# Kernel tuning notes

Measured on AMD Instinct MI355X. Metric: run time of the kernel, lower is better.

The kernel has to match this reference:

```python
import jax, jax.numpy as jnp
import numpy as np
import math

MODEL_DIM = 1024
BATCH = 4
SEQ = 4096
ATTENTION_INPUT = 'both'


def make_F(model_dim, attention_input):
    F = jnp.zeros((model_dim, model_dim), dtype=jnp.float32)
    if attention_input == 'both':
        a = model_dim
    else:
        a = model_dim // 2
    # faithful to source: elif means 'both' only hits the first branch
    if attention_input in ['both', 'only_sem']:
        idx = jnp.arange(0, a)
        F = F.at[idx, idx].set(1.0)
    elif attention_input in ['only_pos']:
        idx = jnp.arange(a, 2 * a)
        F = F.at[idx, idx].set(1.0)
    return F


def setup_inputs() -> dict:
    key = jax.random.key(0)
    kx, kq, kk, kv = jax.random.split(key, 4)
    x = jax.random.normal(kx, (BATCH, SEQ, MODEL_DIM), dtype=jnp.float32)
    Q = jax.random.normal(kq, (MODEL_DIM, MODEL_DIM), dtype=jnp.float32) / math.sqrt(MODEL_DIM)
    K = jax.random.normal(kk, (MODEL_DIM, MODEL_DIM), dtype=jnp.float32) / math.sqrt(MODEL_DIM)
    V = jax.random.normal(kv, (MODEL_DIM, MODEL_DIM), dtype=jnp.float32) / math.sqrt(MODEL_DIM)
    return {"x": x, "Q": Q, "K": K, "V": V}


def reference(x, Q, K, V):
    model_dim = Q.shape[0]
    F = make_F(model_dim, ATTENTION_INPUT)
    Qx = x @ F @ Q            # [B, S, D]
    Kx = x @ F @ K            # [B, S, D]
    Vx = x @ V                # [B, S, D]
    scores = jnp.einsum('bqd,bkd->bqk', Qx, Kx) / math.sqrt(model_dim)  # [B, S, S]
    seq = x.shape[1]
    causal_mask = jnp.triu(jnp.ones((seq, seq), dtype=bool), k=1)       # True above diagonal
    scores = jnp.where(causal_mask, -jnp.inf, scores)
    probs = jax.nn.softmax(scores, axis=-1)
    return jnp.einsum('bqk,bkd->bqd', probs, Vx)
```

## Files before the change

### kernel.cpp

```cpp
#include <hip/hip_runtime.h>
#include <cstdint>
#include <cstddef>
#include <cmath>


typedef unsigned short u16;
typedef __bf16  bf16x8 __attribute__((ext_vector_type(8)));
typedef float   f32x4  __attribute__((ext_vector_type(4)));
typedef unsigned short u16x4 __attribute__((ext_vector_type(4)));
typedef unsigned short u16x8 __attribute__((ext_vector_type(8)));

typedef __attribute__((address_space(1))) void gvoid;
typedef __attribute__((address_space(3))) void lvoid;

__device__ __forceinline__ u16 f2bf(float f) {
  union { float f; unsigned u; } v; v.f = f;
  unsigned u = v.u;
  u += 0x7FFFu + ((u >> 16) & 1u);
  return (u16)(u >> 16);
}
__device__ __forceinline__ float bf2f(u16 h) {
  union { unsigned u; float f; } v; v.u = ((unsigned)h) << 16;
  return v.f;
}
__device__ __forceinline__ void async16(const void* g, void* l) {
  __builtin_amdgcn_global_load_lds((gvoid*)(void*)g, (lvoid*)l, 16, 0, 0);
}

__global__ void __launch_bounds__(256) cvt_f32_bf16(const float4* __restrict__ in,
                                                    u16* __restrict__ out, int n4) {
  int i = blockIdx.x * 256 + threadIdx.x;
  if (i >= n4) return;
  float4 v = in[i];
  u16x4 o = { f2bf(v.x), f2bf(v.y), f2bf(v.z), f2bf(v.w) };
  *(u16x4*)(out + 4 * (size_t)i) = o;
}

template <typename TIN>
__global__ void __launch_bounds__(256) transpose_to_bf16(
    const TIN* __restrict__ in, u16* __restrict__ out,
    int rows, int cols, long inStride, long outStride, float scale) {
  __shared__ u16 t[64][68];
  int rt = blockIdx.x * 64, ct = blockIdx.y * 64;
  long ib = (long)blockIdx.z * inStride, ob = (long)blockIdx.z * outStride;
  int tx = threadIdx.x & 63, ty = threadIdx.x >> 6;
#pragma unroll
  for (int r = ty; r < 64; r += 4)
    t[r][tx] = f2bf((float)in[ib + (long)(rt + r) * cols + ct + tx] * scale);
  __syncthreads();
#pragma unroll
  for (int r = ty; r < 64; r += 4)
    out[ob + (long)(ct + r) * rows + rt + tx] = t[tx][r];
}


#define G8_BAR()  __builtin_amdgcn_s_barrier()
#define G8_VMC4() asm volatile("s_waitcnt vmcnt(4)" ::: "memory")
#define G8_VMC0() asm volatile("s_waitcnt vmcnt(0)" ::: "memory")

#define G8_STAGE_A(bn, kp, kb) do { \
    async16(Ag + (kb) + a0, (void*)&As[bn][kp][l0]); \
    async16(Ag + (kb) + a1, (void*)&As[bn][kp][l1]); } while (0)
#define G8_STAGE_B(bn, kp, kb) do { \
    async16(Bg + (kb) + b0, (void*)&Bs[bn][kp][l0]); \
    async16(Bg + (kb) + b1, (void*)&Bs[bn][kp][l1]); } while (0)

#define G8_LDA(bc, kp, ch) do { _Pragma("unroll") \
    for (int u_ = 0; u_ < 4; ++u_) \
      af[u_] = *(const bf16x8*)&As[bc][kp][(wm * 128 + (ch) * 64 + u_ * 16 + lr) * 32 + swq]; \
  } while (0)
#define G8_LDB(bc, kp) do { _Pragma("unroll") \
    for (int j_ = 0; j_ < 4; ++j_) \
      bf[j_] = *(const bf16x8*)&Bs[bc][kp][(wn * 64 + j_ * 16 + lr) * 32 + swq]; \
  } while (0)

#define G8_MFMA(ch) do { \
    __builtin_amdgcn_s_setprio(1); \
    _Pragma("unroll") for (int u_ = 0; u_ < 4; ++u_) \
      _Pragma("unroll") for (int j_ = 0; j_ < 4; ++j_) \
        acc[(ch) * 4 + u_][j_] = __builtin_amdgcn_mfma_f32_16x16x32_bf16( \
            af[u_], bf[j_], acc[(ch) * 4 + u_][j_], 0, 0, 0); \
    __builtin_amdgcn_s_setprio(0); } while (0)

#define G8_TILE(bc, bn, kt, kn) do { \
    bf16x8 af[4], bf[4]; \
     \
    G8_LDB(bc, 0); G8_LDA(bc, 0, 0); \
    G8_STAGE_A(bn, 0, (kn)); \
    G8_BAR(); G8_MFMA(0); G8_BAR(); \
     \
    G8_LDA(bc, 0, 1); \
    G8_STAGE_B(bn, 0, (kn)); \
    G8_BAR(); G8_MFMA(1); G8_VMC4(); G8_BAR(); \
     \
    G8_LDB(bc, 1); G8_LDA(bc, 1, 0); \
    G8_STAGE_A(bn, 1, (kn) + 32); \
    G8_BAR(); G8_MFMA(0); G8_BAR(); \
     \
    G8_LDA(bc, 1, 1); \
    G8_STAGE_B(bn, 1, (kn) + 32); \
    G8_BAR(); G8_MFMA(1); G8_VMC4(); G8_BAR(); } while (0)

template <bool OUTF32, bool TRI>
__global__ void __launch_bounds__(512, 2) gemm8_bt(
    const u16* __restrict__ A, const u16* __restrict__ Bt, void* __restrict__ C,
    int K, int lda, int ldb, int ldc,
    long aStride, long bStride, long cStride, float alpha) {
  int mt, nt;
  if (TRI) {
    const int bid = blockIdx.x;
    int m = (int)((sqrtf(8.0f * (float)bid + 1.0f) - 1.0f) * 0.5f);
    while ((m + 1) * (m + 2) / 2 <= bid) ++m;
    while (m * (m + 1) / 2 > bid) --m;
    mt = m; nt = bid - m * (m + 1) / 2;
  } else { mt = blockIdx.x; nt = blockIdx.y; }
  const int bz = blockIdx.z;
  const int tid = threadIdx.x, wv = tid >> 6, ln = tid & 63;
  const int wm = wv & 1, wn = wv >> 1;
  const int lr = ln & 15, quad = ln >> 4;
  const int swq = (quad ^ ((lr >> 1) & 3)) << 3;
  const u16* Ag = A + (long)bz * aStride + (long)(mt * 256) * lda;
  const u16* Bg = Bt + (long)bz * bStride + (long)(nt * 256) * ldb;

  __shared__ __align__(16) __bf16 As[2][2][256 * 32];
  __shared__ __align__(16) __bf16 Bs[2][2][256 * 32];

  f32x4 acc[8][4];
#pragma unroll
  for (int i = 0; i < 8; ++i)
#pragma unroll
    for (int j = 0; j < 4; ++j)
#pragma unroll
      for (int r = 0; r < 4; ++r) acc[i][j][r] = 0.f;

  const int c0 = tid, c1 = tid + 512;
  const int r0 = c0 >> 2, r1 = c1 >> 2;
  const long a0 = (long)r0 * lda + (((c0 & 3) ^ ((r0 >> 1) & 3)) << 3);
  const long a1 = (long)r1 * lda + (((c1 & 3) ^ ((r1 >> 1) & 3)) << 3);
  const long b0 = (long)r0 * ldb + (((c0 & 3) ^ ((r0 >> 1) & 3)) << 3);
  const long b1 = (long)r1 * ldb + (((c1 & 3) ^ ((r1 >> 1) & 3)) << 3);
  const int l0 = c0 * 8, l1 = c1 * 8;

  const int kend = K;

  G8_STAGE_A(0, 0, 0); G8_STAGE_B(0, 0, 0);
  G8_STAGE_A(0, 1, 32); G8_STAGE_B(0, 1, 32);
  G8_VMC4(); G8_BAR();

  for (int k0 = 0; k0 < kend; k0 += 128) {
    const long kn0 = (k0 + 64  < kend) ? (long)k0 + 64  : (long)k0;
    const long kn1 = (k0 + 128 < kend) ? (long)k0 + 128 : (long)k0 + 64;
    G8_TILE(0, 1, k0, kn0);
    G8_TILE(1, 0, k0 + 64, kn1);
  }
  G8_VMC0();

  const long cb = (long)bz * cStride;
#pragma unroll
  for (int i = 0; i < 8; ++i) {
    int row0 = mt * 256 + wm * 128 + i * 16 + quad * 4;
#pragma unroll
    for (int j = 0; j < 4; ++j) {
      int col = nt * 256 + wn * 64 + j * 16 + lr;
#pragma unroll
      for (int r = 0; r < 4; ++r) {
        float v = acc[i][j][r] * alpha;
        long idx = cb + (long)(row0 + r) * ldc + col;
        if (OUTF32) ((float*)C)[idx] = v;
        else        ((u16*)C)[idx]  = f2bf(v);
      }
    }
  }
}

template <bool OUTF32, bool TRI, bool CK, int BM>
__global__ void __launch_bounds__(256, BM == 256 ? 2 : 4) gemm_bt(
    const u16* __restrict__ A, const u16* __restrict__ Bt, void* __restrict__ C,
    int K, int lda, int ldb, int ldc,
    long aStride, long bStride, long cStride, float alpha) {
  constexpr int MR = BM / 32;
  constexpr int AQ = BM / 64;
  int mt, nt, bz;
  if (TRI) {
    const int bid = blockIdx.x;
    int m = (int)((sqrtf(4.0f * (float)bid + 1.0f) - 1.0f) * 0.5f);
    while ((m + 1) * (m + 2) <= bid) ++m;
    while (m * (m + 1) > bid) --m;
    mt = m; nt = bid - m * (m + 1);
    bz = blockIdx.z;
  } else if (CK) {
    const int id = blockIdx.x;
    const int g = id & 7, mid = (id >> 3) & 31, hi = id >> 8;
    bz = mid & 3; nt = mid >> 2;
    mt = (hi == 0) ? 31 - g : (hi == 1) ? 16 + g : (hi == 2) ? 15 - g : g;
  } else {
    mt = blockIdx.x; nt = blockIdx.y; bz = blockIdx.z;
  }
  const int tid = threadIdx.x, wv = tid >> 6, ln = tid & 63;
  const u16* Ag = A + (long)bz * aStride + (long)(mt * BM) * lda;
  const u16* Bg = Bt + (long)bz * bStride + (long)(nt * 128) * ldb;

  __shared__ __align__(16) __bf16 As[2][BM * 32];
  __shared__ __align__(16) __bf16 Bs[2][128 * 32];

  f32x4 acc[MR][4];
#pragma unroll
  for (int i = 0; i < MR; ++i)
#pragma unroll
    for (int j = 0; j < 4; ++j)
#pragma unroll
      for (int r = 0; r < 4; ++r) acc[i][j][r] = 0.f;

  const int kend = CK ? (((mt + 1) * BM < K) ? (mt + 1) * BM : K) : K;
  const int wm = wv & 1, wn = wv >> 1;
  const int mrow = wm * (BM / 2), nrow = wn * 64;
  const int lr = ln & 15, quad = ln >> 4;

  long aOff[AQ]; int aLds[AQ];
#pragma unroll
  for (int q = 0; q < AQ; ++q) {
    int c = q * 256 + tid, row = c >> 2, c8i = c & 3;
    aOff[q] = (long)row * lda + ((c8i ^ ((row >> 1) & 3)) << 3);
    aLds[q] = c * 8;
  }
  long bOff[2]; int bLds[2];
#pragma unroll
  for (int q = 0; q < 2; ++q) {
    int c = q * 256 + tid, row = c >> 2, c8i = c & 3;
    bOff[q] = (long)row * ldb + ((c8i ^ ((row >> 1) & 3)) << 3);
    bLds[q] = c * 8;
  }
  const int swq = (quad ^ ((lr >> 1) & 3)) << 3;

  for (int k0 = 0; k0 < kend; k0 += 64) {
#pragma unroll
    for (int p = 0; p < 2; ++p) {
      const long kk = k0 + p * 32;
#pragma unroll
      for (int q = 0; q < AQ; ++q)
        async16(Ag + kk + aOff[q], (char*)As[p] + aLds[q] * 2);
#pragma unroll
      for (int q = 0; q < 2; ++q)
        async16(Bg + kk + bOff[q], (char*)Bs[p] + bLds[q] * 2);
    }
    __syncthreads();
#pragma unroll
    for (int p = 0; p < 2; ++p) {
      bf16x8 af[MR], bfr[4];
#pragma unroll
      for (int u = 0; u < MR; ++u)
        af[u] = *(const bf16x8*)&As[p][(mrow + u * 16 + lr) * 32 + swq];
#pragma unroll
      for (int j = 0; j < 4; ++j)
        bfr[j] = *(const bf16x8*)&Bs[p][(nrow + j * 16 + lr) * 32 + swq];
#pragma unroll
      for (int u = 0; u < MR; ++u)
#pragma unroll
        for (int j = 0; j < 4; ++j)
          acc[u][j] = __builtin_amdgcn_mfma_f32_16x16x32_bf16(af[u], bfr[j], acc[u][j], 0, 0, 0);
    }
    __syncthreads();
  }

  const long cb = (long)bz * cStride;
#pragma unroll
  for (int i = 0; i < MR; ++i) {
    int row0 = mt * BM + mrow + i * 16 + quad * 4;
#pragma unroll
    for (int j = 0; j < 4; ++j) {
      int col = nt * 128 + nrow + j * 16 + lr;
#pragma unroll
      for (int r = 0; r < 4; ++r) {
        float v = acc[i][j][r] * alpha;
        long idx = cb + (long)(row0 + r) * ldc + col;
        if (OUTF32) ((float*)C)[idx] = v;
        else        ((u16*)C)[idx]  = f2bf(v);
      }
    }
  }
}

__global__ void __launch_bounds__(256) softmax_rows(u16* __restrict__ Sb,
                                                    long bStride, int S) {
  const int row = blockIdx.x;
  u16* p = Sb + (long)blockIdx.y * bStride + (long)row * S;
  const int L = row + 1;
  const int Lpad = (L + 255) & ~255;
  const int tid = threadIdx.x, ln = tid & 63, wv = tid >> 6;
  const int base0 = tid * 16;
  __shared__ float red[4];

  float vals[16];
  float lmax = -3.4e38f;
#pragma unroll
  for (int k = 0; k < 2; ++k) {
    const int b = base0 + k * 8;
    if (b < L) {
      u16x8 v = *(const u16x8*)(p + b);
#pragma unroll
      for (int e = 0; e < 8; ++e) {
        if (b + e < L) { float f = bf2f(v[e]); vals[k * 8 + e] = f; lmax = fmaxf(lmax, f); }
        else vals[k * 8 + e] = 0.f;
      }
    } else {
#pragma unroll
      for (int e = 0; e < 8; ++e) vals[k * 8 + e] = 0.f;
    }
  }
#pragma unroll
  for (int o = 32; o > 0; o >>= 1) lmax = fmaxf(lmax, __shfl_down(lmax, o));
  if (ln == 0) red[wv] = lmax;
  __syncthreads();
  float m = fmaxf(fmaxf(red[0], red[1]), fmaxf(red[2], red[3]));

  float lsum = 0.f;
#pragma unroll
  for (int k = 0; k < 2; ++k) {
    const int b = base0 + k * 8;
#pragma unroll
    for (int e = 0; e < 8; ++e) {
      float ex = (b + e < L) ? __expf(vals[k * 8 + e] - m) : 0.f;
      vals[k * 8 + e] = ex; lsum += ex;
    }
  }
#pragma unroll
  for (int o = 32; o > 0; o >>= 1) lsum += __shfl_down(lsum, o);
  __syncthreads();
  if (ln == 0) red[wv] = lsum;
  __syncthreads();
  float inv = 1.f / (red[0] + red[1] + red[2] + red[3]);
#pragma unroll
  for (int k = 0; k < 2; ++k) {
    const int b = base0 + k * 8;
    if (b < Lpad) {
      u16x8 o;
#pragma unroll
      for (int e = 0; e < 8; ++e) o[e] = f2bf(vals[k * 8 + e] * inv);
      *(u16x8*)(p + b) = o;
    }
  }
}

extern "C" void kernel_launch(void* const* d_in, const int* in_sizes, int n_in,
                              void* d_out, int out_size, void* d_ws, size_t ws_size,
                              hipStream_t stream) {
  const float* x = (const float*)d_in[0];
  const float* Q = (const float*)d_in[1];
  const float* K = (const float*)d_in[2];
  const float* V = (const float*)d_in[3];
  float* out = (float*)d_out;

  constexpr int  Bb = 4, S = 4096, D = 1024;
  constexpr long MB = 1024 * 1024;
  if (ws_size < (size_t)(224 * MB)) return;

  char* ws = (char*)d_ws;
  u16* QKx  = (u16*)(ws);
  u16* Vxt  = (u16*)(ws + 64 * MB);
  u16* Sb   = (u16*)(ws + 96 * MB);
  u16* XB   = (u16*)(ws + 128 * MB);
  u16* WTqk = (u16*)(ws + 160 * MB);
  u16* WTv  = (u16*)(ws + 164 * MB);

  const long SD = (long)S * D, SS = (long)S * S;

  cvt_f32_bf16<<<dim3((Bb * S * D / 4) / 256), 256, 0, stream>>>(
      (const float4*)x, XB, Bb * S * D / 4);

  transpose_to_bf16<float><<<dim3(16, 16, 1), 256, 0, stream>>>(
      Q, WTqk, 1024, 1024, 0, 0, 0.03125f);
  transpose_to_bf16<float><<<dim3(16, 16, 1), 256, 0, stream>>>(
      K, WTqk + 1024 * 1024, 1024, 1024, 0, 0, 1.0f);
  transpose_to_bf16<float><<<dim3(16, 16, 1), 256, 0, stream>>>(
      V, WTv, 1024, 1024, 0, 0, 1.0f);

  gemm8_bt<false, false><<<dim3(64, 8, 1), 512, 0, stream>>>(
      XB, WTqk, QKx, 1024, 1024, 1024, 2048, 0, 0, 0, 1.0f);
  gemm8_bt<false, false><<<dim3(4, 64, 1), 512, 0, stream>>>(
      WTv, XB, Vxt, 1024, 1024, 1024, 16384, 0, 0, 0, 1.0f);

  gemm8_bt<false, true><<<dim3(136, 1, Bb), 512, 0, stream>>>(
      QKx, QKx + 1024, Sb, 1024, 2048, 2048, S, 2 * SD, 2 * SD, SS, 1.0f);

  softmax_rows<<<dim3(S, Bb), 256, 0, stream>>>(Sb, SS, S);

  gemm_bt<true, false, true, 128><<<dim3(1024, 1, 1), 256, 0, stream>>>(
      Sb, Vxt, out, S, S, 16384, D, SS, 4096, SD, 1.0f);
}
```

Baseline: 475.4 us.

## Add pipelined 256x128 GEMM kernel for causal scores and PV product

Adds a new 512-thread GEMM kernel with a 256x128 tile. It uses the same double-buffered async-staging pipeline as the existing 256x256 kernel. The causal QK^T score GEMM now runs on this kernel in triangular mode, which gives more blocks and less wasted work on the diagonal. The probs×V GEMM also moves to it, replacing the older 128-row kernel that loaded each tile and then synchronised without overlapping loads and compute. The trade-off is more blocks per launch and a different occupancy and register profile per block.

```diff
diff --git a/kernel.cpp b/kernel.cpp
--- a/kernel.cpp
+++ b/kernel.cpp
@@ -82,39 +82,27 @@
             af[u_], bf[j_], acc[(ch) * 4 + u_][j_], 0, 0, 0); \
     __builtin_amdgcn_s_setprio(0); } while (0)
 
-#define G8_TILE(bc, bn, kt, kn) do { \
+#define G8_TILE(bc, bn, kn) do { \
     bf16x8 af[4], bf[4]; \
-     \
     G8_LDB(bc, 0); G8_LDA(bc, 0, 0); \
     G8_STAGE_A(bn, 0, (kn)); \
     G8_BAR(); G8_MFMA(0); G8_BAR(); \
-     \
     G8_LDA(bc, 0, 1); \
     G8_STAGE_B(bn, 0, (kn)); \
     G8_BAR(); G8_MFMA(1); G8_VMC4(); G8_BAR(); \
-     \
     G8_LDB(bc, 1); G8_LDA(bc, 1, 0); \
     G8_STAGE_A(bn, 1, (kn) + 32); \
     G8_BAR(); G8_MFMA(0); G8_BAR(); \
-     \
     G8_LDA(bc, 1, 1); \
     G8_STAGE_B(bn, 1, (kn) + 32); \
     G8_BAR(); G8_MFMA(1); G8_VMC4(); G8_BAR(); } while (0)
 
-template <bool OUTF32, bool TRI>
+template <bool OUTF32>
 __global__ void __launch_bounds__(512, 2) gemm8_bt(
     const u16* __restrict__ A, const u16* __restrict__ Bt, void* __restrict__ C,
     int K, int lda, int ldb, int ldc,
     long aStride, long bStride, long cStride, float alpha) {
-  int mt, nt;
-  if (TRI) {
-    const int bid = blockIdx.x;
-    int m = (int)((sqrtf(8.0f * (float)bid + 1.0f) - 1.0f) * 0.5f);
-    while ((m + 1) * (m + 2) / 2 <= bid) ++m;
-    while (m * (m + 1) / 2 > bid) --m;
-    mt = m; nt = bid - m * (m + 1) / 2;
-  } else { mt = blockIdx.x; nt = blockIdx.y; }
-  const int bz = blockIdx.z;
+  const int mt = blockIdx.x, nt = blockIdx.y, bz = blockIdx.z;
   const int tid = threadIdx.x, wv = tid >> 6, ln = tid & 63;
   const int wm = wv & 1, wn = wv >> 1;
   const int lr = ln & 15, quad = ln >> 4;
@@ -150,8 +138,8 @@
   for (int k0 = 0; k0 < kend; k0 += 128) {
     const long kn0 = (k0 + 64  < kend) ? (long)k0 + 64  : (long)k0;
     const long kn1 = (k0 + 128 < kend) ? (long)k0 + 128 : (long)k0 + 64;
-    G8_TILE(0, 1, k0, kn0);
-    G8_TILE(1, 0, k0 + 64, kn1);
+    G8_TILE(0, 1, kn0);
+    G8_TILE(1, 0, kn1);
   }
   G8_VMC0();
 
@@ -173,13 +161,52 @@
   }
 }
 
-template <bool OUTF32, bool TRI, bool CK, int BM>
-__global__ void __launch_bounds__(256, BM == 256 ? 2 : 4) gemm_bt(
+
+#define H8_VMC3() asm volatile("s_waitcnt vmcnt(3)" ::: "memory")
+
+#define H8_STAGE_A(bn, kp, kb) do { \
+    async16(Ag + (kb) + a0, (void*)&As[bn][kp][l0]); \
+    async16(Ag + (kb) + a1, (void*)&As[bn][kp][l1]); } while (0)
+#define H8_STAGE_B(bn, kp, kb) \
+    async16(Bg + (kb) + b0, (void*)&Bs[bn][kp][l0])
+
+#define H8_LDA(bc, kp, ch) do { _Pragma("unroll") \
+    for (int u_ = 0; u_ < 2; ++u_) \
+      af[u_] = *(const bf16x8*)&As[bc][kp][(wm * 64 + (ch) * 32 + u_ * 16 + lr) * 32 + swq]; \
+  } while (0)
+#define H8_LDB(bc, kp) do { _Pragma("unroll") \
+    for (int j_ = 0; j_ < 4; ++j_) \
+      bf[j_] = *(const bf16x8*)&Bs[bc][kp][(wn * 64 + j_ * 16 + lr) * 32 + swq]; \
+  } while (0)
+
+#define H8_MFMA(ch) do { \
+    __builtin_amdgcn_s_setprio(1); \
+    _Pragma("unroll") for (int u_ = 0; u_ < 2; ++u_) \
+      _Pragma("unroll") for (int j_ = 0; j_ < 4; ++j_) \
+        acc[(ch) * 2 + u_][j_] = __builtin_amdgcn_mfma_f32_16x16x32_bf16( \
+            af[u_], bf[j_], acc[(ch) * 2 + u_][j_], 0, 0, 0); \
+    __builtin_amdgcn_s_setprio(0); } while (0)
+
+#define H8_TILE(bc, bn, kn) do { \
+    bf16x8 af[2], bf[4]; \
+    H8_LDB(bc, 0); H8_LDA(bc, 0, 0); \
+    H8_STAGE_A(bn, 0, (kn)); \
+    G8_BAR(); H8_MFMA(0); G8_BAR(); \
+    H8_LDA(bc, 0, 1); \
+    H8_STAGE_B(bn, 0, (kn)); \
+    G8_BAR(); H8_MFMA(1); H8_VMC3(); G8_BAR(); \
+    H8_LDB(bc, 1); H8_LDA(bc, 1, 0); \
+    H8_STAGE_A(bn, 1, (kn) + 32); \
+    G8_BAR(); H8_MFMA(0); G8_BAR(); \
+    H8_LDA(bc, 1, 1); \
+    H8_STAGE_B(bn, 1, (kn) + 32); \
+    G8_BAR(); H8_MFMA(1); H8_VMC3(); G8_BAR(); } while (0)
+
+template <bool OUTF32, bool TRI, bool CK>
+__global__ void __launch_bounds__(512, 2) gemm8h_bt(
     const u16* __restrict__ A, const u16* __restrict__ Bt, void* __restrict__ C,
     int K, int lda, int ldb, int ldc,
     long aStride, long bStride, long cStride, float alpha) {
-  constexpr int MR = BM / 32;
-  constexpr int AQ = BM / 64;
   int mt, nt, bz;
   if (TRI) {
     const int bid = blockIdx.x;
@@ -190,85 +217,56 @@
     bz = blockIdx.z;
   } else if (CK) {
     const int id = blockIdx.x;
-    const int g = id & 7, mid = (id >> 3) & 31, hi = id >> 8;
-    bz = mid & 3; nt = mid >> 2;
-    mt = (hi == 0) ? 31 - g : (hi == 1) ? 16 + g : (hi == 2) ? 15 - g : g;
+    mt = 15 - (id >> 5); bz = id & 3; nt = (id >> 2) & 7;
   } else {
     mt = blockIdx.x; nt = blockIdx.y; bz = blockIdx.z;
   }
   const int tid = threadIdx.x, wv = tid >> 6, ln = tid & 63;
-  const u16* Ag = A + (long)bz * aStride + (long)(mt * BM) * lda;
+  const int wm = wv & 3, wn = wv >> 2;
+  const int lr = ln & 15, quad = ln >> 4;
+  const int swq = (quad ^ ((lr >> 1) & 3)) << 3;
+  const u16* Ag = A + (long)bz * aStride + (long)(mt * 256) * lda;
   const u16* Bg = Bt + (long)bz * bStride + (long)(nt * 128) * ldb;
 
-  __shared__ __align__(16) __bf16 As[2][BM * 32];
-  __shared__ __align__(16) __bf16 Bs[2][128 * 32];
-
-  f32x4 acc[MR][4];
-#pragma unroll
-  for (int i = 0; i < MR; ++i)
+  __shared__ __align__(16) __bf16 As[2][2][256 * 32];
+  __shared__ __align__(16) __bf16 Bs[2][2][128 * 32];
+
+  f32x4 acc[4][4];
+#pragma unroll
+  for (int i = 0; i < 4; ++i)
 #pragma unroll
     for (int j = 0; j < 4; ++j)
 #pragma unroll
       for (int r = 0; r < 4; ++r) acc[i][j][r] = 0.f;
 
-  const int kend = CK ? (((mt + 1) * BM < K) ? (mt + 1) * BM : K) : K;
-  const int wm = wv & 1, wn = wv >> 1;
-  const int mrow = wm * (BM / 2), nrow = wn * 64;
-  const int lr = ln & 15, quad = ln >> 4;
-
-  long aOff[AQ]; int aLds[AQ];
-#pragma unroll
-  for (int q = 0; q < AQ; ++q) {
-    int c = q * 256 + tid, row = c >> 2, c8i = c & 3;
-    aOff[q] = (long)row * lda + ((c8i ^ ((row >> 1) & 3)) << 3);
-    aLds[q] = c * 8;
-  }
-  long bOff[2]; int bLds[2];
-#pragma unroll
-  for (int q = 0; q < 2; ++q) {
-    int c = q * 256 + tid, row = c >> 2, c8i = c & 3;
-    bOff[q] = (long)row * ldb + ((c8i ^ ((row >> 1) & 3)) << 3);
-    bLds[q] = c * 8;
-  }
-  const int swq = (quad ^ ((lr >> 1) & 3)) << 3;
-
-  for (int k0 = 0; k0 < kend; k0 += 64) {
-#pragma unroll
-    for (int p = 0; p < 2; ++p) {
-      const long kk = k0 + p * 32;
-#pragma unroll
-      for (int q = 0; q < AQ; ++q)
-        async16(Ag + kk + aOff[q], (char*)As[p] + aLds[q] * 2);
-#pragma unroll
-      for (int q = 0; q < 2; ++q)
-        async16(Bg + kk + bOff[q], (char*)Bs[p] + bLds[q] * 2);
-    }
-    __syncthreads();
-#pragma unroll
-    for (int p = 0; p < 2; ++p) {
-      bf16x8 af[MR], bfr[4];
-#pragma unroll
-      for (int u = 0; u < MR; ++u)
-        af[u] = *(const bf16x8*)&As[p][(mrow + u * 16 + lr) * 32 + swq];
-#pragma unroll
-      for (int j = 0; j < 4; ++j)
-        bfr[j] = *(const bf16x8*)&Bs[p][(nrow + j * 16 + lr) * 32 + swq];
-#pragma unroll
-      for (int u = 0; u < MR; ++u)
-#pragma unroll
-        for (int j = 0; j < 4; ++j)
-          acc[u][j] = __builtin_amdgcn_mfma_f32_16x16x32_bf16(af[u], bfr[j], acc[u][j], 0, 0, 0);
-    }
-    __syncthreads();
-  }
+  const int c0 = tid, c1 = tid + 512;
+  const int r0 = c0 >> 2, r1 = c1 >> 2;
+  const long a0 = (long)r0 * lda + (((c0 & 3) ^ ((r0 >> 1) & 3)) << 3);
+  const long a1 = (long)r1 * lda + (((c1 & 3) ^ ((r1 >> 1) & 3)) << 3);
+  const long b0 = (long)r0 * ldb + (((c0 & 3) ^ ((r0 >> 1) & 3)) << 3);
+  const int l0 = c0 * 8, l1 = c1 * 8;
+
+  const int kend = CK ? (((mt + 1) * 256 < K) ? (mt + 1) * 256 : K) : K;
+
+  H8_STAGE_A(0, 0, 0); H8_STAGE_B(0, 0, 0);
+  H8_STAGE_A(0, 1, 32); H8_STAGE_B(0, 1, 32);
+  H8_VMC3(); G8_BAR();
+
+  for (int k0 = 0; k0 < kend; k0 += 128) {
+    const long kn0 = (k0 + 64  < kend) ? (long)k0 + 64  : (long)k0;
+    const long kn1 = (k0 + 128 < kend) ? (long)k0 + 128 : (long)k0 + 64;
+    H8_TILE(0, 1, kn0);
+    H8_TILE(1, 0, kn1);
+  }
+  G8_VMC0();
 
   const long cb = (long)bz * cStride;
 #pragma unroll
-  for (int i = 0; i < MR; ++i) {
-    int row0 = mt * BM + mrow + i * 16 + quad * 4;
+  for (int i = 0; i < 4; ++i) {
+    int row0 = mt * 256 + wm * 64 + i * 16 + quad * 4;
 #pragma unroll
     for (int j = 0; j < 4; ++j) {
-      int col = nt * 128 + nrow + j * 16 + lr;
+      int col = nt * 128 + wn * 64 + j * 16 + lr;
 #pragma unroll
       for (int r = 0; r < 4; ++r) {
         float v = acc[i][j][r] * alpha;
@@ -374,16 +372,16 @@
   transpose_to_bf16<float><<<dim3(16, 16, 1), 256, 0, stream>>>(
       V, WTv, 1024, 1024, 0, 0, 1.0f);
 
-  gemm8_bt<false, false><<<dim3(64, 8, 1), 512, 0, stream>>>(
+  gemm8_bt<false><<<dim3(64, 8, 1), 512, 0, stream>>>(
       XB, WTqk, QKx, 1024, 1024, 1024, 2048, 0, 0, 0, 1.0f);
-  gemm8_bt<false, false><<<dim3(4, 64, 1), 512, 0, stream>>>(
+  gemm8_bt<false><<<dim3(4, 64, 1), 512, 0, stream>>>(
       WTv, XB, Vxt, 1024, 1024, 1024, 16384, 0, 0, 0, 1.0f);
 
-  gemm8_bt<false, true><<<dim3(136, 1, Bb), 512, 0, stream>>>(
+  gemm8h_bt<false, true, false><<<dim3(272, 1, Bb), 512, 0, stream>>>(
       QKx, QKx + 1024, Sb, 1024, 2048, 2048, S, 2 * SD, 2 * SD, SS, 1.0f);
 
   softmax_rows<<<dim3(S, Bb), 256, 0, stream>>>(Sb, SS, S);
 
-  gemm_bt<true, false, true, 128><<<dim3(1024, 1, 1), 256, 0, stream>>>(
+  gemm8h_bt<true, false, true><<<dim3(512, 1, 1), 512, 0, stream>>>(
       Sb, Vxt, out, S, S, 16384, D, SS, 4096, SD, 1.0f);
 }
```

After: 491.9 us. 3.5% more time.
